# Optimization experiments

Measured on AMD Instinct MI355X. Metric: run time of the kernel, lower is better.

Reference implementation:

```python
import jax, jax.numpy as jnp
import numpy as np

N, E = 50000, 800000
IN_CH, HID, MSG_HID, L = 128, 256, 128, 10
EPS = 1e-5


def _xavier(key, shape):
    fan_in, fan_out = shape[-2], shape[-1]
    lim = np.sqrt(6.0 / (fan_in + fan_out))
    return jax.random.uniform(key, shape, jnp.float32, -lim, lim)


def setup_inputs() -> dict:
    key = jax.random.key(0)
    ks = jax.random.split(key, 10)
    x = jax.random.normal(ks[0], (N, IN_CH), jnp.float32)
    edge_index = jax.random.randint(ks[1], (2, E), 0, N, jnp.int32)
    Win = _xavier(ks[2], (IN_CH, HID))
    bin_ = jnp.zeros((HID,), jnp.float32)
    # per-layer stacked params [L, ...]
    W1 = _xavier(ks[3], (L, HID, MSG_HID))
    b1 = jnp.zeros((L, MSG_HID), jnp.float32)
    W2 = _xavier(ks[4], (L, MSG_HID, HID))
    b2 = jnp.zeros((L, HID), jnp.float32)
    U1 = _xavier(ks[5], (L, HID, HID))
    c1 = jnp.zeros((L, HID), jnp.float32)
    U2 = _xavier(ks[6], (L, HID, HID))
    c2 = jnp.zeros((L, HID), jnp.float32)
    ln_g = jnp.ones((L, HID), jnp.float32)
    ln_b = jnp.zeros((L, HID), jnp.float32)
    beta = 0.01 * jax.random.normal(ks[7], (L + 1,), jnp.float32)
    return {"x": x, "edge_index": edge_index, "Win": Win, "bin_": bin_,
            "W1": W1, "b1": b1, "W2": W2, "b2": b2,
            "U1": U1, "c1": c1, "U2": U2, "c2": c2,
            "ln_g": ln_g, "ln_b": ln_b, "beta": beta}


def reference(x, edge_index, Win, bin_, W1, b1, W2, b2, U1, c1, U2, c2, ln_g, ln_b, beta):
    n = x.shape[0]
    self_loop = jnp.arange(n, dtype=edge_index.dtype)
    src = jnp.concatenate([edge_index[0], self_loop])  # x_j (source)
    dst = jnp.concatenate([edge_index[1], self_loop])  # aggregate at target i
    counts = jax.ops.segment_sum(jnp.ones_like(dst, dtype=x.dtype), dst, num_segments=n)
    counts = counts[:, None]  # >=1 thanks to self loops

    z0 = x @ Win + bin_  # input_lin, use_activation=False

    def layer(z, p):
        w1, bb1, w2, bb2, u1, cc1, u2, cc2, g, b_ = p
        msg = jax.nn.relu(z[src] @ w1 + bb1) @ w2 + bb2       # [E+N, HID]
        m = jax.ops.segment_sum(msg, dst, num_segments=n) / counts
        h = z + m
        out = jax.nn.relu(h @ u1 + cc1) @ u2 + cc2
        mu = out.mean(-1, keepdims=True)
        var = out.var(-1, keepdims=True)
        out = (out - mu) * jax.lax.rsqrt(var + EPS) * g + b_
        return out, out

    _, zs = jax.lax.scan(layer, z0, (W1, b1, W2, b2, U1, c1, U2, c2, ln_g, ln_b))
    zs_all = jnp.concatenate([z0[None], zs], axis=0)  # [L+1, N, HID]
    betas = jax.nn.softmax(beta)
    return jnp.einsum('l,lnh->nh', betas, zs_all)
```

## Files before the change

kernel.cpp:

```cpp
#include <hip/hip_runtime.h>
#include <stdint.h>

typedef __attribute__((ext_vector_type(4))) float f32x4;
typedef __attribute__((ext_vector_type(8))) short bf16x8;

#define HIDC 256
#define MSGC 128
#define NLAYER 10

__device__ __forceinline__ ushort f2bf(float f) {
  union { float f; uint32_t u; } a; a.f = f;
  uint32_t u = a.u;
  return (ushort)((u + 0x7fffu + ((u >> 16) & 1u)) >> 16);
}
__device__ __forceinline__ float bf2f(ushort h) {
  union { float f; uint32_t u; } a; a.u = ((uint32_t)h) << 16;
  return a.f;
}

__global__ __launch_bounds__(256, 4) void gemm_w1(
    const ushort* __restrict__ A, const ushort* __restrict__ B,
    const float* __restrict__ bias, ushort* __restrict__ C, int M) {
  __shared__ ushort lA[128 * 64];
  __shared__ ushort lB[128 * 64];
  const int tid = threadIdx.x;
  const int m0 = blockIdx.x * 128;
  const int lane = tid & 63;
  const int w = tid >> 6;
  const int wm = (w >> 1) * 64;
  const int wn = (w & 1) * 64;
  const int rr = tid >> 3;
  const int cc = tid & 7;
  f32x4 acc[4][4] = {};

#pragma unroll
  for (int s = 0; s < 4; ++s) {
    const int k0 = s * 64;
#pragma unroll
    for (int p = 0; p < 4; ++p) {
      const int row = p * 32 + rr;
      const int gm = m0 + row;
      bf16x8 av = {0, 0, 0, 0, 0, 0, 0, 0};
      if (gm < M) av = *(const bf16x8*)(A + (size_t)gm * 256 + k0 + cc * 8);
      const uint32_t off = (uint32_t)((row * 128 + cc * 16) ^ ((row & 7) << 4));
      *(bf16x8*)((char*)lA + off) = av;
    }
#pragma unroll
    for (int p = 0; p < 4; ++p) {
      const int row = p * 32 + rr;
      bf16x8 bv = *(const bf16x8*)(B + (size_t)row * 256 + k0 + cc * 8);
      const uint32_t off = (uint32_t)((row * 128 + cc * 16) ^ ((row & 7) << 4));
      *(bf16x8*)((char*)lB + off) = bv;
    }
    __syncthreads();
#pragma unroll
    for (int kk = 0; kk < 2; ++kk) {
      bf16x8 ah[4];
#pragma unroll
      for (int i = 0; i < 4; ++i) {
        const int arow = wm + i * 16 + (lane & 15);
        const uint32_t ao =
            (uint32_t)((arow * 128 + kk * 64 + ((lane >> 4) * 16)) ^ ((arow & 7) << 4));
        ah[i] = *(const bf16x8*)((const char*)lA + ao);
      }
#pragma unroll
      for (int j = 0; j < 4; ++j) {
        const int brow = wn + j * 16 + (lane & 15);
        const uint32_t bo =
            (uint32_t)((brow * 128 + kk * 64 + ((lane >> 4) * 16)) ^ ((brow & 7) << 4));
        const bf16x8 bv = *(const bf16x8*)((const char*)lB + bo);
#pragma unroll
        for (int i = 0; i < 4; ++i)
          acc[i][j] = __builtin_amdgcn_mfma_f32_16x16x32_bf16(ah[i], bv, acc[i][j], 0, 0, 0);
      }
    }
    __syncthreads();
  }
  float bi[4];
#pragma unroll
  for (int j = 0; j < 4; ++j) bi[j] = bias[wn + j * 16 + (lane & 15)];
#pragma unroll
  for (int i = 0; i < 4; ++i) {
    const int gm0 = m0 + wm + i * 16 + ((lane >> 4) << 2);
#pragma unroll
    for (int r = 0; r < 4; ++r) {
      const int gm = gm0 + r;
      if (gm < M) {
        const size_t base = (size_t)gm * 128 + wn + (lane & 15);
#pragma unroll
        for (int j = 0; j < 4; ++j)
          C[base + j * 16] = f2bf(fmaxf(acc[i][j][r] + bi[j], 0.f));
      }
    }
  }
}

template <int RELU, int ADDZ, int LN>
__global__ __launch_bounds__(512, 4) void gemm_big(
    const ushort* __restrict__ A, const ushort* __restrict__ B,
    const float* __restrict__ bias, const ushort* __restrict__ Z,
    ushort* __restrict__ C, const float* __restrict__ g,
    const float* __restrict__ b_, int M, int K) {
  __shared__ ushort lA[128 * 64];
  __shared__ ushort lB[256 * 64];
  __shared__ float sstat[2][4][128];
  const int tid = threadIdx.x;
  const int m0 = blockIdx.x * 128;
  const int lane = tid & 63;
  const int w = tid >> 6;
  const int wm = (w >> 2) * 64;
  const int wn = (w & 3) * 64;
  const int rr = tid >> 3;
  const int cc = tid & 7;
  f32x4 acc[4][4] = {};

  const int nsteps = K >> 6;
  for (int s = 0; s < nsteps; ++s) {
    const int k0 = s * 64;
#pragma unroll
    for (int p = 0; p < 2; ++p) {
      const int row = p * 64 + rr;
      const int gm = m0 + row;
      bf16x8 av = {0, 0, 0, 0, 0, 0, 0, 0};
      if (gm < M) av = *(const bf16x8*)(A + (size_t)gm * K + k0 + cc * 8);
      const uint32_t off = (uint32_t)((row * 128 + cc * 16) ^ ((row & 7) << 4));
      *(bf16x8*)((char*)lA + off) = av;
    }
#pragma unroll
    for (int p = 0; p < 4; ++p) {
      const int row = p * 64 + rr;
      bf16x8 bv = *(const bf16x8*)(B + (size_t)row * K + k0 + cc * 8);
      const uint32_t off = (uint32_t)((row * 128 + cc * 16) ^ ((row & 7) << 4));
      *(bf16x8*)((char*)lB + off) = bv;
    }
    __syncthreads();
#pragma unroll
    for (int kk = 0; kk < 2; ++kk) {
      bf16x8 ah[4];
#pragma unroll
      for (int i = 0; i < 4; ++i) {
        const int arow = wm + i * 16 + (lane & 15);
        const uint32_t ao =
            (uint32_t)((arow * 128 + kk * 64 + ((lane >> 4) * 16)) ^ ((arow & 7) << 4));
        ah[i] = *(const bf16x8*)((const char*)lA + ao);
      }
#pragma unroll
      for (int j = 0; j < 4; ++j) {
        const int brow = wn + j * 16 + (lane & 15);
        const uint32_t bo =
            (uint32_t)((brow * 128 + kk * 64 + ((lane >> 4) * 16)) ^ ((brow & 7) << 4));
        const bf16x8 bv = *(const bf16x8*)((const char*)lB + bo);
#pragma unroll
        for (int i = 0; i < 4; ++i)
          acc[i][j] = __builtin_amdgcn_mfma_f32_16x16x32_bf16(ah[i], bv, acc[i][j], 0, 0, 0);
      }
    }
    __syncthreads();
  }

  float bi[4];
#pragma unroll
  for (int j = 0; j < 4; ++j) bi[j] = bias[wn + j * 16 + (lane & 15)];

  if (LN) {
    float gv[4], bv[4];
#pragma unroll
    for (int j = 0; j < 4; ++j) {
      gv[j] = g[wn + j * 16 + (lane & 15)];
      bv[j] = b_[wn + j * 16 + (lane & 15)];
    }
#pragma unroll
    for (int i = 0; i < 4; ++i) {
#pragma unroll
      for (int r = 0; r < 4; ++r) {
        float s1 = 0.f, s2 = 0.f;
#pragma unroll
        for (int j = 0; j < 4; ++j) {
          float v = acc[i][j][r] + bi[j];
          acc[i][j][r] = v;
          s1 += v;
          s2 += v * v;
        }
#pragma unroll
        for (int d = 1; d < 16; d <<= 1) {
          s1 += __shfl_xor(s1, d);
          s2 += __shfl_xor(s2, d);
        }
        if ((lane & 15) == 0) {
          const int rl = wm + i * 16 + ((lane >> 4) << 2) + r;
          sstat[0][w & 3][rl] = s1;
          sstat[1][w & 3][rl] = s2;
        }
      }
    }
    __syncthreads();
#pragma unroll
    for (int i = 0; i < 4; ++i) {
#pragma unroll
      for (int r = 0; r < 4; ++r) {
        const int rl = wm + i * 16 + ((lane >> 4) << 2) + r;
        const float s1 = sstat[0][0][rl] + sstat[0][1][rl] + sstat[0][2][rl] + sstat[0][3][rl];
        const float s2 = sstat[1][0][rl] + sstat[1][1][rl] + sstat[1][2][rl] + sstat[1][3][rl];
        const float mu = s1 * (1.f / 256.f);
        const float var = s2 * (1.f / 256.f) - mu * mu;
        const float rs = rsqrtf(var + 1e-5f);
        const int gm = m0 + rl;
        if (gm < M) {
          const size_t base = (size_t)gm * 256 + wn + (lane & 15);
#pragma unroll
          for (int j = 0; j < 4; ++j)
            C[base + j * 16] = f2bf((acc[i][j][r] - mu) * rs * gv[j] + bv[j]);
        }
      }
    }
  } else {
#pragma unroll
    for (int i = 0; i < 4; ++i) {
      const int gm0 = m0 + wm + i * 16 + ((lane >> 4) << 2);
#pragma unroll
      for (int r = 0; r < 4; ++r) {
        const int gm = gm0 + r;
        if (gm < M) {
          const size_t base = (size_t)gm * 256 + wn + (lane & 15);
#pragma unroll
          for (int j = 0; j < 4; ++j) {
            float v = acc[i][j][r] + bi[j];
            if (ADDZ) v += bf2f(Z[base + j * 16]);
            if (RELU) v = fmaxf(v, 0.f);
            C[base + j * 16] = f2bf(v);
          }
        }
      }
    }
  }
}

template <int WRITE>
__global__ __launch_bounds__(256) void fold_kernel(
    const ushort* __restrict__ zbase, size_t ZS, const float* __restrict__ betas,
    int l0, int P, float* __restrict__ outp, int total8) {
  const int i = blockIdx.x * 256 + threadIdx.x;
  if (i >= total8) return;
  float a[8] = {};
  for (int k = 0; k < P; ++k) {
    const float bl = betas[l0 + k];
    const uint4 u = ((const uint4*)(zbase + k * ZS))[i];
    const uint32_t ww[4] = {u.x, u.y, u.z, u.w};
#pragma unroll
    for (int q = 0; q < 4; ++q) {
      union { uint32_t u; float f; } lo, hi;
      lo.u = ww[q] << 16;
      hi.u = ww[q] & 0xffff0000u;
      a[2 * q] += bl * lo.f;
      a[2 * q + 1] += bl * hi.f;
    }
  }
  f32x4 o0 = {a[0], a[1], a[2], a[3]};
  f32x4 o1 = {a[4], a[5], a[6], a[7]};
  if (WRITE) {
    ((f32x4*)outp)[(size_t)i * 2] = o0;
    ((f32x4*)outp)[(size_t)i * 2 + 1] = o1;
  } else {
    f32x4 p0 = ((f32x4*)outp)[(size_t)i * 2];
    f32x4 p1 = ((f32x4*)outp)[(size_t)i * 2 + 1];
    ((f32x4*)outp)[(size_t)i * 2] = p0 + o0;
    ((f32x4*)outp)[(size_t)i * 2 + 1] = p1 + o1;
  }
}

__global__ void count_kernel(const int* __restrict__ dstv, int* __restrict__ deg, int E) {
  int i = blockIdx.x * 256 + threadIdx.x;
  if (i < E) atomicAdd(&deg[dstv[i]], 1);
}

__global__ void scanA_kernel(const int* __restrict__ deg, int* __restrict__ excl,
                             int* __restrict__ bsum, int n) {
  __shared__ int sm[256];
  const int i = blockIdx.x * 256 + threadIdx.x;
  const int v = (i < n) ? deg[i] : 0;
  sm[threadIdx.x] = v;
  __syncthreads();
  for (int off = 1; off < 256; off <<= 1) {
    int t = (threadIdx.x >= off) ? sm[threadIdx.x - off] : 0;
    __syncthreads();
    sm[threadIdx.x] += t;
    __syncthreads();
  }
  if (i < n) excl[i] = sm[threadIdx.x] - v;
  if (threadIdx.x == 255) bsum[blockIdx.x] = sm[255];
}

__global__ void scanB_kernel(const int* __restrict__ bsum, int* __restrict__ boff, int nb) {
  __shared__ int sm[256];
  const int v = (threadIdx.x < nb) ? bsum[threadIdx.x] : 0;
  sm[threadIdx.x] = v;
  __syncthreads();
  for (int off = 1; off < 256; off <<= 1) {
    int t = (threadIdx.x >= off) ? sm[threadIdx.x - off] : 0;
    __syncthreads();
    sm[threadIdx.x] += t;
    __syncthreads();
  }
  if (threadIdx.x < nb) boff[threadIdx.x] = sm[threadIdx.x] - v;
}

__global__ void scanC_kernel(const int* __restrict__ deg, const int* __restrict__ excl,
                             const int* __restrict__ boff, int* __restrict__ rowptr,
                             int* __restrict__ fillptr, float* __restrict__ invc,
                             int n, int E) {
  const int i = blockIdx.x * 256 + threadIdx.x;
  if (i < n) {
    const int r = excl[i] + boff[blockIdx.x];
    rowptr[i] = r;
    fillptr[i] = r;
    invc[i] = 1.0f / (float)(deg[i] + 1);
  }
  if (i == 0) rowptr[n] = E;
}

__global__ void fill_kernel(const int* __restrict__ srcv, const int* __restrict__ dstv,
                            int* __restrict__ fillptr, int* __restrict__ colv, int E) {
  int i = blockIdx.x * 256 + threadIdx.x;
  if (i < E) {
    int p = atomicAdd(&fillptr[dstv[i]], 1);
    colv[p] = srcv[i];
  }
}

__global__ __launch_bounds__(256) void agg128_kernel(
    const uint32_t* __restrict__ T, const int* __restrict__ rowptr,
    const int* __restrict__ colv, const float* __restrict__ invc,
    uint32_t* __restrict__ sout, int n) {
  const int node = blockIdx.x * 4 + (threadIdx.x >> 6);
  if (node >= n) return;
  const int lane = threadIdx.x & 63;
  auto up0 = [](uint32_t u) {
    union { uint32_t u; float f; } a; a.u = u << 16; return a.f;
  };
  auto up1 = [](uint32_t u) {
    union { uint32_t u; float f; } a; a.u = u & 0xffff0000u; return a.f;
  };
  const uint32_t self = T[(size_t)node * 64 + lane];
  float a0 = up0(self), a1 = up1(self);
  float b0 = 0.f, b1 = 0.f, c0 = 0.f, c1 = 0.f, d0 = 0.f, d1 = 0.f;
  const int s = rowptr[node];
  const int e = rowptr[node + 1];
  int i = s;
  for (; i + 3 < e; i += 4) {
    const int s0 = colv[i], s1 = colv[i + 1], s2 = colv[i + 2], s3 = colv[i + 3];
    const uint32_t u0 = T[(size_t)s0 * 64 + lane];
    const uint32_t u1 = T[(size_t)s1 * 64 + lane];
    const uint32_t u2 = T[(size_t)s2 * 64 + lane];
    const uint32_t u3 = T[(size_t)s3 * 64 + lane];
    a0 += up0(u0); a1 += up1(u0);
    b0 += up0(u1); b1 += up1(u1);
    c0 += up0(u2); c1 += up1(u2);
    d0 += up0(u3); d1 += up1(u3);
  }
  for (; i < e; ++i) {
    const uint32_t u0 = T[(size_t)colv[i] * 64 + lane];
    a0 += up0(u0); a1 += up1(u0);
  }
  const float ic = invc[node];
  const float r0 = (a0 + b0 + c0 + d0) * ic;
  const float r1 = (a1 + b1 + c1 + d1) * ic;
  sout[(size_t)node * 64 + lane] = (uint32_t)f2bf(r0) | ((uint32_t)f2bf(r1) << 16);
}

__global__ void beta_kernel(const float* __restrict__ beta, float* __restrict__ betas) {
  if (threadIdx.x == 0) {
    float mx = beta[0];
    for (int i = 1; i < NLAYER + 1; ++i) mx = fmaxf(mx, beta[i]);
    float e[NLAYER + 1];
    float s = 0.f;
    for (int i = 0; i < NLAYER + 1; ++i) {
      e[i] = expf(beta[i] - mx);
      s += e[i];
    }
    const float inv = 1.f / s;
    for (int i = 0; i < NLAYER + 1; ++i) betas[i] = e[i] * inv;
  }
}

__global__ void wconv_kernel(const float* __restrict__ W, ushort* __restrict__ Wt,
                             int K, int Nn) {
  const size_t matoff = (size_t)blockIdx.z * K * Nn;
  const int o = blockIdx.x * 256 + threadIdx.x;
  if (o >= K * Nn) return;
  const int nn = o / K;
  const int kk = o - nn * K;
  Wt[matoff + o] = f2bf(W[matoff + (size_t)kk * Nn + nn]);
}

__global__ void xcast_kernel(const float* __restrict__ x, ushort* __restrict__ xb, int n8) {
  const int i = blockIdx.x * 256 + threadIdx.x;
  if (i >= n8) return;
  const f32x4 v0 = ((const f32x4*)x)[(size_t)i * 2];
  const f32x4 v1 = ((const f32x4*)x)[(size_t)i * 2 + 1];
  bf16x8 o;
#pragma unroll
  for (int q = 0; q < 4; ++q) {
    o[q] = (short)f2bf(v0[q]);
    o[q + 4] = (short)f2bf(v1[q]);
  }
  *(bf16x8*)(xb + (size_t)i * 8) = o;
}

extern "C" void kernel_launch(void* const* d_in, const int* in_sizes, int n_in,
                              void* d_out, int out_size, void* d_ws, size_t ws_size,
                              hipStream_t stream) {
  const float* x = (const float*)d_in[0];
  const int* eidx = (const int*)d_in[1];
  const float* Win = (const float*)d_in[2];
  const float* bin_ = (const float*)d_in[3];
  const float* W1 = (const float*)d_in[4];
  const float* b1 = (const float*)d_in[5];
  const float* W2 = (const float*)d_in[6];
  const float* b2 = (const float*)d_in[7];
  const float* U1 = (const float*)d_in[8];
  const float* c1 = (const float*)d_in[9];
  const float* U2 = (const float*)d_in[10];
  const float* c2 = (const float*)d_in[11];
  const float* ln_g = (const float*)d_in[12];
  const float* ln_b = (const float*)d_in[13];
  const float* beta = (const float*)d_in[14];
  float* outp = (float*)d_out;

  const int Nn = in_sizes[0] / 128;
  const int E = in_sizes[1] / 2;
  const int* srcv = eidx;
  const int* dstv = eidx + E;

  char* p = (char*)d_ws;
  auto alloc = [&](size_t bytes) {
    char* r = p;
    p += (bytes + 255) & ~(size_t)255;
    return r;
  };
  ushort* hbuf = (ushort*)alloc((size_t)Nn * HIDC * 2);
  ushort* TSO = (ushort*)alloc((size_t)Nn * HIDC * 2);
  ushort* xbf = (ushort*)alloc((size_t)Nn * 128 * 2);
  ushort* WinT = (ushort*)alloc(128 * 256 * 2);
  ushort* W1T = (ushort*)alloc((size_t)NLAYER * 256 * 128 * 2);
  ushort* W2T = (ushort*)alloc((size_t)NLAYER * 128 * 256 * 2);
  ushort* U1T = (ushort*)alloc((size_t)NLAYER * 256 * 256 * 2);
  ushort* U2T = (ushort*)alloc((size_t)NLAYER * 256 * 256 * 2);
  int* deg = (int*)alloc((size_t)Nn * 4);
  int* rowptr = (int*)alloc((size_t)(Nn + 1) * 4);
  int* fillptr = (int*)alloc((size_t)Nn * 4);
  float* invc = (float*)alloc((size_t)Nn * 4);
  int* colv = (int*)alloc((size_t)E * 4);
  int* excl = (int*)alloc((size_t)Nn * 4);
  int* bsum = (int*)alloc(256 * 4);
  int* boff = (int*)alloc(256 * 4);
  float* betas = (float*)alloc(64);

  const size_t ZS = (size_t)Nn * HIDC;
  const size_t slotB = ZS * 2;
  const size_t used = (size_t)(p - (char*)d_ws);
  int G = 2;
  if (ws_size > used + 4096) {
    size_t fit = (ws_size - used - 4096) / (slotB + 256);
    G = (int)(fit < 2 ? 2 : (fit > NLAYER + 1 ? NLAYER + 1 : fit));
  }
  ushort* zbase = (ushort*)alloc((size_t)G * slotB);

  ushort* T128 = TSO;
  ushort* s128 = TSO + (size_t)Nn * MSGC;
  ushort* Obuf = TSO;

  const int nscan = (Nn + 255) / 256;
  const int mb128 = (Nn + 127) / 128;
  const int nwave = (Nn + 3) / 4;
  const int total8 = (Nn * HIDC) / 8;

  hipMemsetAsync(deg, 0, (size_t)Nn * 4, stream);
  count_kernel<<<(E + 255) / 256, 256, 0, stream>>>(dstv, deg, E);
  scanA_kernel<<<nscan, 256, 0, stream>>>(deg, excl, bsum, Nn);
  scanB_kernel<<<1, 256, 0, stream>>>(bsum, boff, nscan);
  scanC_kernel<<<nscan, 256, 0, stream>>>(deg, excl, boff, rowptr, fillptr, invc, Nn, E);
  fill_kernel<<<(E + 255) / 256, 256, 0, stream>>>(srcv, dstv, fillptr, colv, E);
  beta_kernel<<<1, 64, 0, stream>>>(beta, betas);
  xcast_kernel<<<(Nn * 16 + 255) / 256, 256, 0, stream>>>(x, xbf, Nn * 16);
  wconv_kernel<<<dim3(128, 1, 1), 256, 0, stream>>>(Win, WinT, 128, 256);
  wconv_kernel<<<dim3(128, 1, NLAYER), 256, 0, stream>>>(W1, W1T, 256, 128);
  wconv_kernel<<<dim3(128, 1, NLAYER), 256, 0, stream>>>(W2, W2T, 128, 256);
  wconv_kernel<<<dim3(256, 1, NLAYER), 256, 0, stream>>>(U1, U1T, 256, 256);
  wconv_kernel<<<dim3(256, 1, NLAYER), 256, 0, stream>>>(U2, U2T, 256, 256);

  int pend = 0, l0 = 0;
  bool first = true;
  auto flush = [&]() {
    if (pend > 0) {
      if (first)
        fold_kernel<1><<<(total8 + 255) / 256, 256, 0, stream>>>(zbase, ZS, betas, l0,
                                                                 pend, outp, total8);
      else
        fold_kernel<0><<<(total8 + 255) / 256, 256, 0, stream>>>(zbase, ZS, betas, l0,
                                                                 pend, outp, total8);
      first = false;
      l0 += pend;
      pend = 0;
    }
  };

  ushort* zcur = zbase;
  gemm_big<0, 0, 0><<<mb128, 512, 0, stream>>>(xbf, WinT, bin_, nullptr, zcur, nullptr,
                                               nullptr, Nn, 128);
  pend = 1;

  for (int l = 0; l < NLAYER; ++l) {
    gemm_w1<<<mb128, 256, 0, stream>>>(zcur, W1T + (size_t)l * 256 * 128, b1 + l * 128,
                                       T128, Nn);
    agg128_kernel<<<nwave, 256, 0, stream>>>((const uint32_t*)T128, rowptr, colv, invc,
                                             (uint32_t*)s128, Nn);
    gemm_big<0, 1, 0><<<mb128, 512, 0, stream>>>(s128, W2T + (size_t)l * 128 * 256,
                                                 b2 + l * 256, zcur, hbuf, nullptr,
                                                 nullptr, Nn, 128);
    gemm_big<1, 0, 0><<<mb128, 512, 0, stream>>>(hbuf, U1T + (size_t)l * 256 * 256,
                                                 c1 + l * 256, nullptr, Obuf, nullptr,
                                                 nullptr, Nn, 256);
    if (pend == G) flush();
    ushort* znext = zbase + (size_t)pend * slotB / 2;
    gemm_big<0, 0, 1><<<mb128, 512, 0, stream>>>(Obuf, U2T + (size_t)l * 256 * 256,
                                                 c2 + l * 256, nullptr, znext,
                                                 ln_g + l * 256, ln_b + l * 256, Nn, 256);
    zcur = znext;
    pend++;
  }
  flush();
}
```

Measured before the change: 1.464 ms.

## Fuse W2, U1, U2 GEMMs and layernorm into one per-layer kernel

Replaces the three per-layer gemm_big launches (W2+residual, U1+relu, U2+layernorm) with a single layer_fused kernel that keeps the 64-row intermediate activations in shared memory. This removes the global round trips for the h and O buffers. It also widens agg128 to 16-byte gathers with 16 lanes per node, and has count/fill handle 4 edges per thread. In exchange the tile shrinks to 64 rows, there is more LDS per block (lower occupancy), and each block reloads all three weight matrices.

```diff
diff --git a/kernel.cpp b/kernel.cpp
--- a/kernel.cpp
+++ b/kernel.cpp
@@ -95,15 +95,11 @@
   }
 }
 
-template <int RELU, int ADDZ, int LN>
-__global__ __launch_bounds__(512, 4) void gemm_big(
+__global__ __launch_bounds__(512, 4) void gemm_win(
     const ushort* __restrict__ A, const ushort* __restrict__ B,
-    const float* __restrict__ bias, const ushort* __restrict__ Z,
-    ushort* __restrict__ C, const float* __restrict__ g,
-    const float* __restrict__ b_, int M, int K) {
+    const float* __restrict__ bias, ushort* __restrict__ C, int M) {
   __shared__ ushort lA[128 * 64];
   __shared__ ushort lB[256 * 64];
-  __shared__ float sstat[2][4][128];
   const int tid = threadIdx.x;
   const int m0 = blockIdx.x * 128;
   const int lane = tid & 63;
@@ -113,9 +109,10 @@
   const int rr = tid >> 3;
   const int cc = tid & 7;
   f32x4 acc[4][4] = {};
-
-  const int nsteps = K >> 6;
-  for (int s = 0; s < nsteps; ++s) {
+  const int K = 128;
+
+#pragma unroll
+  for (int s = 0; s < 2; ++s) {
     const int k0 = s * 64;
 #pragma unroll
     for (int p = 0; p < 2; ++p) {
@@ -157,20 +154,222 @@
     }
     __syncthreads();
   }
-
   float bi[4];
 #pragma unroll
   for (int j = 0; j < 4; ++j) bi[j] = bias[wn + j * 16 + (lane & 15)];
-
-  if (LN) {
-    float gv[4], bv[4];
+#pragma unroll
+  for (int i = 0; i < 4; ++i) {
+    const int gm0 = m0 + wm + i * 16 + ((lane >> 4) << 2);
+#pragma unroll
+    for (int r = 0; r < 4; ++r) {
+      const int gm = gm0 + r;
+      if (gm < M) {
+        const size_t base = (size_t)gm * 256 + wn + (lane & 15);
+#pragma unroll
+        for (int j = 0; j < 4; ++j)
+          C[base + j * 16] = f2bf(acc[i][j][r] + bi[j]);
+      }
+    }
+  }
+}
+
+__global__ __launch_bounds__(512, 4) void layer_fused(
+    const ushort* __restrict__ s128, const ushort* __restrict__ z,
+    const ushort* __restrict__ W2T, const float* __restrict__ b2,
+    const ushort* __restrict__ U1T, const float* __restrict__ c1,
+    const ushort* __restrict__ U2T, const float* __restrict__ c2,
+    const float* __restrict__ g, const float* __restrict__ b_,
+    ushort* __restrict__ zout, int M) {
+  __shared__ ushort lA[64 * 64];
+  __shared__ ushort lB[256 * 64];
+  __shared__ ushort hO[64 * 256];
+  __shared__ float sstat[2][4][64];
+  const int tid = threadIdx.x;
+  const int m0 = blockIdx.x * 64;
+  const int lane = tid & 63;
+  const int w = tid >> 6;
+  const int wm = (w >> 2) * 32;
+  const int wn = (w & 3) * 64;
+  const int rr = tid >> 3;
+  const int cc = tid & 7;
+  f32x4 acc[2][4];
+
+#pragma unroll
+  for (int i = 0; i < 2; ++i)
+#pragma unroll
+    for (int j = 0; j < 4; ++j) acc[i][j] = (f32x4){0.f, 0.f, 0.f, 0.f};
+#pragma unroll
+  for (int s = 0; s < 2; ++s) {
+    const int k0 = s * 64;
+    {
+      const int gm = m0 + rr;
+      bf16x8 av = {0, 0, 0, 0, 0, 0, 0, 0};
+      if (gm < M) av = *(const bf16x8*)(s128 + (size_t)gm * 128 + k0 + cc * 8);
+      const uint32_t off = (uint32_t)((rr * 128 + cc * 16) ^ ((rr & 7) << 4));
+      *(bf16x8*)((char*)lA + off) = av;
+    }
+#pragma unroll
+    for (int p = 0; p < 4; ++p) {
+      const int row = p * 64 + rr;
+      bf16x8 bv = *(const bf16x8*)(W2T + (size_t)row * 128 + k0 + cc * 8);
+      const uint32_t off = (uint32_t)((row * 128 + cc * 16) ^ ((row & 7) << 4));
+      *(bf16x8*)((char*)lB + off) = bv;
+    }
+    __syncthreads();
+#pragma unroll
+    for (int kk = 0; kk < 2; ++kk) {
+      bf16x8 ah[2];
+#pragma unroll
+      for (int i = 0; i < 2; ++i) {
+        const int arow = wm + i * 16 + (lane & 15);
+        const uint32_t ao =
+            (uint32_t)((arow * 128 + kk * 64 + ((lane >> 4) * 16)) ^ ((arow & 7) << 4));
+        ah[i] = *(const bf16x8*)((const char*)lA + ao);
+      }
+#pragma unroll
+      for (int j = 0; j < 4; ++j) {
+        const int brow = wn + j * 16 + (lane & 15);
+        const uint32_t bo =
+            (uint32_t)((brow * 128 + kk * 64 + ((lane >> 4) * 16)) ^ ((brow & 7) << 4));
+        const bf16x8 bv = *(const bf16x8*)((const char*)lB + bo);
+#pragma unroll
+        for (int i = 0; i < 2; ++i)
+          acc[i][j] = __builtin_amdgcn_mfma_f32_16x16x32_bf16(ah[i], bv, acc[i][j], 0, 0, 0);
+      }
+    }
+    __syncthreads();
+  }
+  {
+    float bi[4];
+#pragma unroll
+    for (int j = 0; j < 4; ++j) bi[j] = b2[wn + j * 16 + (lane & 15)];
+#pragma unroll
+    for (int i = 0; i < 2; ++i) {
+#pragma unroll
+      for (int r = 0; r < 4; ++r) {
+        const int rl = wm + i * 16 + ((lane >> 4) << 2) + r;
+        const int gm = m0 + rl;
+#pragma unroll
+        for (int j = 0; j < 4; ++j) {
+          const int col = wn + j * 16 + (lane & 15);
+          float v = acc[i][j][r] + bi[j];
+          if (gm < M) v += bf2f(z[(size_t)gm * 256 + col]);
+          const uint32_t off = (uint32_t)((rl * 512 + col * 2) ^ ((rl & 7) << 4));
+          *(ushort*)((char*)hO + off) = f2bf(v);
+        }
+      }
+    }
+  }
+  __syncthreads();
+
+#pragma unroll
+  for (int i = 0; i < 2; ++i)
+#pragma unroll
+    for (int j = 0; j < 4; ++j) acc[i][j] = (f32x4){0.f, 0.f, 0.f, 0.f};
+#pragma unroll
+  for (int s = 0; s < 4; ++s) {
+    const int k0 = s * 64;
+#pragma unroll
+    for (int p = 0; p < 4; ++p) {
+      const int row = p * 64 + rr;
+      bf16x8 bv = *(const bf16x8*)(U1T + (size_t)row * 256 + k0 + cc * 8);
+      const uint32_t off = (uint32_t)((row * 128 + cc * 16) ^ ((row & 7) << 4));
+      *(bf16x8*)((char*)lB + off) = bv;
+    }
+    __syncthreads();
+#pragma unroll
+    for (int kk = 0; kk < 2; ++kk) {
+      bf16x8 ah[2];
+#pragma unroll
+      for (int i = 0; i < 2; ++i) {
+        const int arow = wm + i * 16 + (lane & 15);
+        const uint32_t ao =
+            (uint32_t)((arow * 512 + k0 * 2 + kk * 64 + ((lane >> 4) * 16)) ^ ((arow & 7) << 4));
+        ah[i] = *(const bf16x8*)((const char*)hO + ao);
+      }
+#pragma unroll
+      for (int j = 0; j < 4; ++j) {
+        const int brow = wn + j * 16 + (lane & 15);
+        const uint32_t bo =
+            (uint32_t)((brow * 128 + kk * 64 + ((lane >> 4) * 16)) ^ ((brow & 7) << 4));
+        const bf16x8 bv = *(const bf16x8*)((const char*)lB + bo);
+#pragma unroll
+        for (int i = 0; i < 2; ++i)
+          acc[i][j] = __builtin_amdgcn_mfma_f32_16x16x32_bf16(ah[i], bv, acc[i][j], 0, 0, 0);
+      }
+    }
+    __syncthreads();
+  }
+  {
+    float bi[4];
+#pragma unroll
+    for (int j = 0; j < 4; ++j) bi[j] = c1[wn + j * 16 + (lane & 15)];
+#pragma unroll
+    for (int i = 0; i < 2; ++i) {
+#pragma unroll
+      for (int r = 0; r < 4; ++r) {
+        const int rl = wm + i * 16 + ((lane >> 4) << 2) + r;
+#pragma unroll
+        for (int j = 0; j < 4; ++j) {
+          const int col = wn + j * 16 + (lane & 15);
+          const float v = fmaxf(acc[i][j][r] + bi[j], 0.f);
+          const uint32_t off = (uint32_t)((rl * 512 + col * 2) ^ ((rl & 7) << 4));
+          *(ushort*)((char*)hO + off) = f2bf(v);
+        }
+      }
+    }
+  }
+  __syncthreads();
+
+#pragma unroll
+  for (int i = 0; i < 2; ++i)
+#pragma unroll
+    for (int j = 0; j < 4; ++j) acc[i][j] = (f32x4){0.f, 0.f, 0.f, 0.f};
+#pragma unroll
+  for (int s = 0; s < 4; ++s) {
+    const int k0 = s * 64;
+#pragma unroll
+    for (int p = 0; p < 4; ++p) {
+      const int row = p * 64 + rr;
+      bf16x8 bv = *(const bf16x8*)(U2T + (size_t)row * 256 + k0 + cc * 8);
+      const uint32_t off = (uint32_t)((row * 128 + cc * 16) ^ ((row & 7) << 4));
+      *(bf16x8*)((char*)lB + off) = bv;
+    }
+    __syncthreads();
+#pragma unroll
+    for (int kk = 0; kk < 2; ++kk) {
+      bf16x8 ah[2];
+#pragma unroll
+      for (int i = 0; i < 2; ++i) {
+        const int arow = wm + i * 16 + (lane & 15);
+        const uint32_t ao =
+            (uint32_t)((arow * 512 + k0 * 2 + kk * 64 + ((lane >> 4) * 16)) ^ ((arow & 7) << 4));
+        ah[i] = *(const bf16x8*)((const char*)hO + ao);
+      }
+#pragma unroll
+      for (int j = 0; j < 4; ++j) {
+        const int brow = wn + j * 16 + (lane & 15);
+        const uint32_t bo =
+            (uint32_t)((brow * 128 + kk * 64 + ((lane >> 4) * 16)) ^ ((brow & 7) << 4));
+        const bf16x8 bv = *(const bf16x8*)((const char*)lB + bo);
+#pragma unroll
+        for (int i = 0; i < 2; ++i)
+          acc[i][j] = __builtin_amdgcn_mfma_f32_16x16x32_bf16(ah[i], bv, acc[i][j], 0, 0, 0);
+      }
+    }
+    __syncthreads();
+  }
+  {
+    float bi[4], gv[4], bv[4];
 #pragma unroll
     for (int j = 0; j < 4; ++j) {
-      gv[j] = g[wn + j * 16 + (lane & 15)];
-      bv[j] = b_[wn + j * 16 + (lane & 15)];
-    }
-#pragma unroll
-    for (int i = 0; i < 4; ++i) {
+      const int col = wn + j * 16 + (lane & 15);
+      bi[j] = c2[col];
+      gv[j] = g[col];
+      bv[j] = b_[col];
+    }
+#pragma unroll
+    for (int i = 0; i < 2; ++i) {
 #pragma unroll
       for (int r = 0; r < 4; ++r) {
         float s1 = 0.f, s2 = 0.f;
@@ -195,7 +394,7 @@
     }
     __syncthreads();
 #pragma unroll
-    for (int i = 0; i < 4; ++i) {
+    for (int i = 0; i < 2; ++i) {
 #pragma unroll
       for (int r = 0; r < 4; ++r) {
         const int rl = wm + i * 16 + ((lane >> 4) << 2) + r;
@@ -209,26 +408,7 @@
           const size_t base = (size_t)gm * 256 + wn + (lane & 15);
 #pragma unroll
           for (int j = 0; j < 4; ++j)
-            C[base + j * 16] = f2bf((acc[i][j][r] - mu) * rs * gv[j] + bv[j]);
-        }
-      }
-    }
-  } else {
-#pragma unroll
-    for (int i = 0; i < 4; ++i) {
-      const int gm0 = m0 + wm + i * 16 + ((lane >> 4) << 2);
-#pragma unroll
-      for (int r = 0; r < 4; ++r) {
-        const int gm = gm0 + r;
-        if (gm < M) {
-          const size_t base = (size_t)gm * 256 + wn + (lane & 15);
-#pragma unroll
-          for (int j = 0; j < 4; ++j) {
-            float v = acc[i][j][r] + bi[j];
-            if (ADDZ) v += bf2f(Z[base + j * 16]);
-            if (RELU) v = fmaxf(v, 0.f);
-            C[base + j * 16] = f2bf(v);
-          }
+            zout[base + j * 16] = f2bf((acc[i][j][r] - mu) * rs * gv[j] + bv[j]);
         }
       }
     }
@@ -269,8 +449,10 @@
 }
 
 __global__ void count_kernel(const int* __restrict__ dstv, int* __restrict__ deg, int E) {
-  int i = blockIdx.x * 256 + threadIdx.x;
-  if (i < E) atomicAdd(&deg[dstv[i]], 1);
+  const int i = (blockIdx.x * 256 + threadIdx.x) * 4;
+#pragma unroll
+  for (int k = 0; k < 4; ++k)
+    if (i + k < E) atomicAdd(&deg[dstv[i + k]], 1);
 }
 
 __global__ void scanA_kernel(const int* __restrict__ deg, int* __restrict__ excl,
@@ -320,51 +502,60 @@
 
 __global__ void fill_kernel(const int* __restrict__ srcv, const int* __restrict__ dstv,
                             int* __restrict__ fillptr, int* __restrict__ colv, int E) {
-  int i = blockIdx.x * 256 + threadIdx.x;
-  if (i < E) {
-    int p = atomicAdd(&fillptr[dstv[i]], 1);
-    colv[p] = srcv[i];
-  }
+  const int i = (blockIdx.x * 256 + threadIdx.x) * 4;
+#pragma unroll
+  for (int k = 0; k < 4; ++k)
+    if (i + k < E) {
+      int p = atomicAdd(&fillptr[dstv[i + k]], 1);
+      colv[p] = srcv[i + k];
+    }
 }
 
 __global__ __launch_bounds__(256) void agg128_kernel(
-    const uint32_t* __restrict__ T, const int* __restrict__ rowptr,
+    const ushort* __restrict__ T, const int* __restrict__ rowptr,
     const int* __restrict__ colv, const float* __restrict__ invc,
-    uint32_t* __restrict__ sout, int n) {
-  const int node = blockIdx.x * 4 + (threadIdx.x >> 6);
+    ushort* __restrict__ sout, int n) {
+  const int node = blockIdx.x * 16 + (threadIdx.x >> 4);
   if (node >= n) return;
-  const int lane = threadIdx.x & 63;
-  auto up0 = [](uint32_t u) {
-    union { uint32_t u; float f; } a; a.u = u << 16; return a.f;
+  const int q = threadIdx.x & 15;
+  const uint4* Tv = (const uint4*)T;
+  float a[8] = {}, b[8] = {}, c[8] = {}, d[8] = {};
+  auto addu = [](float* acc, uint4 u) {
+    const uint32_t ww[4] = {u.x, u.y, u.z, u.w};
+#pragma unroll
+    for (int k = 0; k < 4; ++k) {
+      union { uint32_t u; float f; } lo, hi;
+      lo.u = ww[k] << 16;
+      hi.u = ww[k] & 0xffff0000u;
+      acc[2 * k] += lo.f;
+      acc[2 * k + 1] += hi.f;
+    }
   };
-  auto up1 = [](uint32_t u) {
-    union { uint32_t u; float f; } a; a.u = u & 0xffff0000u; return a.f;
-  };
-  const uint32_t self = T[(size_t)node * 64 + lane];
-  float a0 = up0(self), a1 = up1(self);
-  float b0 = 0.f, b1 = 0.f, c0 = 0.f, c1 = 0.f, d0 = 0.f, d1 = 0.f;
+  addu(a, Tv[(size_t)node * 16 + q]);
   const int s = rowptr[node];
   const int e = rowptr[node + 1];
   int i = s;
   for (; i + 3 < e; i += 4) {
-    const int s0 = colv[i], s1 = colv[i + 1], s2 = colv[i + 2], s3 = colv[i + 3];
-    const uint32_t u0 = T[(size_t)s0 * 64 + lane];
-    const uint32_t u1 = T[(size_t)s1 * 64 + lane];
-    const uint32_t u2 = T[(size_t)s2 * 64 + lane];
-    const uint32_t u3 = T[(size_t)s3 * 64 + lane];
-    a0 += up0(u0); a1 += up1(u0);
-    b0 += up0(u1); b1 += up1(u1);
-    c0 += up0(u2); c1 += up1(u2);
-    d0 += up0(u3); d1 += up1(u3);
-  }
-  for (; i < e; ++i) {
-    const uint32_t u0 = T[(size_t)colv[i] * 64 + lane];
-    a0 += up0(u0); a1 += up1(u0);
-  }
+    const uint4 u0 = Tv[(size_t)colv[i] * 16 + q];
+    const uint4 u1 = Tv[(size_t)colv[i + 1] * 16 + q];
+    const uint4 u2 = Tv[(size_t)colv[i + 2] * 16 + q];
+    const uint4 u3 = Tv[(size_t)colv[i + 3] * 16 + q];
+    addu(a, u0);
+    addu(b, u1);
+    addu(c, u2);
+    addu(d, u3);
+  }
+  for (; i < e; ++i) addu(a, Tv[(size_t)colv[i] * 16 + q]);
   const float ic = invc[node];
-  const float r0 = (a0 + b0 + c0 + d0) * ic;
-  const float r1 = (a1 + b1 + c1 + d1) * ic;
-  sout[(size_t)node * 64 + lane] = (uint32_t)f2bf(r0) | ((uint32_t)f2bf(r1) << 16);
+  uint4 o;
+  uint32_t* ow = (uint32_t*)&o;
+#pragma unroll
+  for (int k = 0; k < 4; ++k) {
+    const float r0 = (a[2 * k] + b[2 * k] + c[2 * k] + d[2 * k]) * ic;
+    const float r1 = (a[2 * k + 1] + b[2 * k + 1] + c[2 * k + 1] + d[2 * k + 1]) * ic;
+    ow[k] = (uint32_t)f2bf(r0) | ((uint32_t)f2bf(r1) << 16);
+  }
+  ((uint4*)sout)[(size_t)node * 16 + q] = o;
 }
 
 __global__ void beta_kernel(const float* __restrict__ beta, float* __restrict__ betas) {
@@ -437,7 +628,6 @@
     p += (bytes + 255) & ~(size_t)255;
     return r;
   };
-  ushort* hbuf = (ushort*)alloc((size_t)Nn * HIDC * 2);
   ushort* TSO = (ushort*)alloc((size_t)Nn * HIDC * 2);
   ushort* xbf = (ushort*)alloc((size_t)Nn * 128 * 2);
   ushort* WinT = (ushort*)alloc(128 * 256 * 2);
@@ -467,19 +657,19 @@
 
   ushort* T128 = TSO;
   ushort* s128 = TSO + (size_t)Nn * MSGC;
-  ushort* Obuf = TSO;
 
   const int nscan = (Nn + 255) / 256;
   const int mb128 = (Nn + 127) / 128;
-  const int nwave = (Nn + 3) / 4;
+  const int mb64 = (Nn + 63) / 64;
+  const int nagg = (Nn + 15) / 16;
   const int total8 = (Nn * HIDC) / 8;
 
   hipMemsetAsync(deg, 0, (size_t)Nn * 4, stream);
-  count_kernel<<<(E + 255) / 256, 256, 0, stream>>>(dstv, deg, E);
+  count_kernel<<<(E + 1023) / 1024, 256, 0, stream>>>(dstv, deg, E);
   scanA_kernel<<<nscan, 256, 0, stream>>>(deg, excl, bsum, Nn);
   scanB_kernel<<<1, 256, 0, stream>>>(bsum, boff, nscan);
   scanC_kernel<<<nscan, 256, 0, stream>>>(deg, excl, boff, rowptr, fillptr, invc, Nn, E);
-  fill_kernel<<<(E + 255) / 256, 256, 0, stream>>>(srcv, dstv, fillptr, colv, E);
+  fill_kernel<<<(E + 1023) / 1024, 256, 0, stream>>>(srcv, dstv, fillptr, colv, E);
   beta_kernel<<<1, 64, 0, stream>>>(beta, betas);
   xcast_kernel<<<(Nn * 16 + 255) / 256, 256, 0, stream>>>(x, xbf, Nn * 16);
   wconv_kernel<<<dim3(128, 1, 1), 256, 0, stream>>>(Win, WinT, 128, 256);
@@ -505,26 +695,19 @@
   };
 
   ushort* zcur = zbase;
-  gemm_big<0, 0, 0><<<mb128, 512, 0, stream>>>(xbf, WinT, bin_, nullptr, zcur, nullptr,
-                                               nullptr, Nn, 128);
+  gemm_win<<<mb128, 512, 0, stream>>>(xbf, WinT, bin_, zcur, Nn);
   pend = 1;
 
   for (int l = 0; l < NLAYER; ++l) {
     gemm_w1<<<mb128, 256, 0, stream>>>(zcur, W1T + (size_t)l * 256 * 128, b1 + l * 128,
                                        T128, Nn);
-    agg128_kernel<<<nwave, 256, 0, stream>>>((const uint32_t*)T128, rowptr, colv, invc,
-                                             (uint32_t*)s128, Nn);
-    gemm_big<0, 1, 0><<<mb128, 512, 0, stream>>>(s128, W2T + (size_t)l * 128 * 256,
-                                                 b2 + l * 256, zcur, hbuf, nullptr,
-                                                 nullptr, Nn, 128);
-    gemm_big<1, 0, 0><<<mb128, 512, 0, stream>>>(hbuf, U1T + (size_t)l * 256 * 256,
-                                                 c1 + l * 256, nullptr, Obuf, nullptr,
-                                                 nullptr, Nn, 256);
+    agg128_kernel<<<nagg, 256, 0, stream>>>(T128, rowptr, colv, invc, s128, Nn);
     if (pend == G) flush();
-    ushort* znext = zbase + (size_t)pend * slotB / 2;
-    gemm_big<0, 0, 1><<<mb128, 512, 0, stream>>>(Obuf, U2T + (size_t)l * 256 * 256,
-                                                 c2 + l * 256, nullptr, znext,
-                                                 ln_g + l * 256, ln_b + l * 256, Nn, 256);
+    ushort* znext = zbase + (size_t)pend * ZS;
+    layer_fused<<<mb64, 512, 0, stream>>>(
+        s128, zcur, W2T + (size_t)l * 128 * 256, b2 + l * 256,
+        U1T + (size_t)l * 256 * 256, c1 + l * 256, U2T + (size_t)l * 256 * 256,
+        c2 + l * 256, ln_g + l * 256, ln_b + l * 256, znext, Nn);
     zcur = znext;
     pend++;
   }
```

Result: no change. 1.467 ms (+0.2%).
